# Performance work log

Measured on AMD Instinct MI355X. Metric: run time of the kernel, lower is better.

The kernel has to match this reference:

```python
import jax, jax.numpy as jnp
import numpy as np

B, N, F_IN, F_OUT, H = 4, 2048, 64, 64, 4

def setup_inputs() -> dict:
    key = jax.random.key(0)
    k1, k2, k3, k4 = jax.random.split(key, 4)
    node_features = jax.random.normal(k1, (B, N, F_IN), dtype=jnp.float32)
    adj_matrix = jax.random.randint(k2, (B, N, N), 0, 2, dtype=jnp.int32)
    # nn.Linear(in, H*out, bias=False): stored here as [in, H*out] so y = x @ W
    W = jax.random.normal(k3, (F_IN, H * F_OUT), dtype=jnp.float32) * (1.0 / np.sqrt(F_IN))
    # per-head additive-attention vector over concatenated [h_i || h_j] (width 2*F_OUT)
    attention = jax.random.normal(k4, (H, 2 * F_OUT), dtype=jnp.float32) * 0.1
    return {"node_features": node_features, "adj_matrix": adj_matrix, "W": W, "attention": attention}

def reference(node_features, adj_matrix, W, attention):
    Bv, Nv = node_features.shape[0], node_features.shape[1]
    # h: [B, H, N, F_OUT]
    h = (node_features @ W).reshape(Bv, Nv, H, F_OUT).transpose(0, 2, 1, 3)
    # Additive GAT scores: a_h . [h_i || h_j] decomposed so the [B,H,N,N,2F] concat
    # tensor is never materialized (same math as concat + einsum in the source).
    a_src, a_dst = attention[:, :F_OUT], attention[:, F_OUT:]
    s_src = jnp.einsum('bhnf,hf->bhn', h, a_src)
    s_dst = jnp.einsum('bhnf,hf->bhn', h, a_dst)
    scores = s_src[:, :, :, None] + s_dst[:, :, None, :]          # [B,H,N,N]
    scores = jnp.where(scores >= 0, scores, 0.2 * scores)          # LeakyReLU(0.2)
    mask = adj_matrix[:, None, :, :].astype(bool)                  # [B,1,N,N]
    scores = jnp.where(mask, scores, -jnp.inf)                     # masked_fill(~mask, -inf)
    attn = jax.nn.softmax(scores, axis=-1)                         # softmax over neighbors j
    # dropout is identity in eval mode (deterministic reference)
    h_prime = jnp.einsum('bhij,bhjf->bhif', attn, h)               # weighted neighbor sum
    return h_prime.transpose(0, 2, 1, 3).reshape(Bv, Nv, H * F_OUT)
```

## Files before the change

### kernel.cpp

```cpp
#include <hip/hip_runtime.h>

#define NN 2048
#define NH 4
#define COLS 256

typedef __attribute__((ext_vector_type(8))) short short8;
typedef __attribute__((ext_vector_type(4))) float f32x4;
typedef __attribute__((ext_vector_type(4))) int i32x4;
typedef __attribute__((ext_vector_type(4))) unsigned u32x4;

__device__ __forceinline__ unsigned cvtpk(float lo, float hi) {
  unsigned r;
  asm("v_cvt_pk_bf16_f32 %0, %1, %2" : "=v"(r) : "v"(lo), "v"(hi));
  return r;
}
__device__ __forceinline__ unsigned pack16(i32x4 a, i32x4 b, i32x4 c, i32x4 d) {
  unsigned m = 0;
  #pragma unroll
  for (int e = 0; e < 4; ++e) {
    m |= (a[e] != 0 ? 1u : 0u) << e;
    m |= (b[e] != 0 ? 1u : 0u) << (e + 4);
    m |= (c[e] != 0 ? 1u : 0u) << (e + 8);
    m |= (d[e] != 0 ? 1u : 0u) << (e + 12);
  }
  return m;
}

__global__ __launch_bounds__(256) void k1_prep(
    const float* __restrict__ nf, const float* __restrict__ W,
    const float* __restrict__ att, ushort* __restrict__ hB,
    float* __restrict__ s_src, float* __restrict__ s_dst)
{
  const int tid = threadIdx.x;
  const int head = tid >> 6, lane = tid & 63;
  const int bid = blockIdx.x;
  const int m0 = bid * 8;

  float w[64];
  #pragma unroll
  for (int f = 0; f < 64; ++f) w[f] = W[f * COLS + tid];

  const float LOG2E = 1.4426950408889634f;
  const float asrc = att[head * 128 + lane] * LOG2E;
  const float adst = att[head * 128 + 64 + lane] * LOG2E;

  __shared__ float xs[512];
  xs[tid]       = nf[m0 * 64 + tid];
  xs[tid + 256] = nf[m0 * 64 + 256 + tid];
  __syncthreads();

  float hv[8];
  #pragma unroll
  for (int rr = 0; rr < 8; ++rr) {
    float acc = 0.f;
    #pragma unroll
    for (int f = 0; f < 64; ++f) acc = fmaf(xs[rr * 64 + f], w[f], acc);
    hv[rr] = acc;
    float vs = acc * asrc, vd = acc * adst;
    #pragma unroll
    for (int off = 32; off > 0; off >>= 1) {
      vs += __shfl_xor(vs, off);
      vd += __shfl_xor(vd, off);
    }
    if (lane == 0) {
      const int m = m0 + rr;
      const int b = m >> 11, n = m & (NN - 1);
      s_src[(b * NH + head) * NN + n] = vs;
      s_dst[(b * NH + head) * NN + n] = vd;
    }
  }

  const int b   = m0 >> 11;
  const int n0  = m0 & (NN - 1);
  const int jc  = n0 >> 5;
  const int grp = (n0 >> 3) & 3;
  const int t   = (tid >> 4) & 3, fl = tid & 15;
  uint4 vv;
  vv.x = cvtpk(hv[0], hv[1]);
  vv.y = cvtpk(hv[2], hv[3]);
  vv.z = cvtpk(hv[4], hv[5]);
  vv.w = cvtpk(hv[6], hv[7]);
  const size_t chunk =
      (((size_t)(b * NH + head) * 64 + jc) * 4 + t) * 64 + (grp * 16 + fl);
  *(uint4*)(hB + chunk * 8) = vv;
}

__global__ __launch_bounds__(512) void k2_main(
    const int* __restrict__ adj, const ushort* __restrict__ hB,
    const float* __restrict__ s_src, const float* __restrict__ s_dst,
    float* __restrict__ out)
{
  const int tid = threadIdx.x;
  const int wv  = tid >> 6;
  const int h   = wv >> 1;
  const int js  = wv & 1;
  const int l   = tid & 63;
  const int L   = blockIdx.x;
  const int b    = (L & 7) >> 1;
  const int iblk = ((L >> 3) << 1) + (L & 1);
  const int i0   = iblk << 4;

  const int bh   = b * NH + h;
  const int r16  = l & 15;
  const int grp  = l >> 4;
  const int koff = grp << 3;

  __shared__ unsigned abits[16][65];
  __shared__ float red[NH][5][4][64];

  {
    const int srow = tid >> 5, sseg = tid & 31;
    const int* sb = adj + ((size_t)(b * NN + i0 + srow)) * NN + sseg * 64;
    unsigned m[4];
    #pragma unroll
    for (int q = 0; q < 4; ++q) {
      const i32x4 a0 = *(const i32x4*)(sb + q * 16);
      const i32x4 a1 = *(const i32x4*)(sb + q * 16 + 4);
      const i32x4 a2 = *(const i32x4*)(sb + q * 16 + 8);
      const i32x4 a3 = *(const i32x4*)(sb + q * 16 + 12);
      m[q] = pack16(a0, a1, a2, a3);
    }
    abits[srow][sseg * 2]     = m[0] | (m[1] << 16);
    abits[srow][sseg * 2 + 1] = m[2] | (m[3] << 16);
  }
  __syncthreads();

  const float ssl = s_src[bh * NN + i0 + r16];
  const float*  sdp = s_dst + bh * NN;
  const ushort* hbW = hB + (size_t)bh * 131072 + l * 8;

  const short8 ones = {(short)0x3F80, (short)0x3F80, (short)0x3F80, (short)0x3F80,
                       (short)0x3F80, (short)0x3F80, (short)0x3F80, (short)0x3F80};

  f32x4 acc[4];
  #pragma unroll
  for (int q = 0; q < 4; ++q) acc[q] = (f32x4){0.f, 0.f, 0.f, 0.f};
  f32x4 acd = (f32x4){0.f, 0.f, 0.f, 0.f};

  #pragma unroll 2
  for (int jc = js * 32; jc < js * 32 + 32; ++jc) {
    const unsigned msk = abits[r16][jc] >> koff;
    const int jb = jc * 32 + koff;
    const f32x4 sd0 = *(const f32x4*)(sdp + jb);
    const f32x4 sd1 = *(const f32x4*)(sdp + jb + 4);
    const ushort* hc = hbW + jc * 2048;
    const short8 hb0 = *(const short8*)(hc);
    const short8 hb1 = *(const short8*)(hc + 512);
    const short8 hb2 = *(const short8*)(hc + 1024);
    const short8 hb3 = *(const short8*)(hc + 1536);

    float pl[8];
    #pragma unroll
    for (int e = 0; e < 8; ++e) {
      const float sdv = (e < 4) ? sd0[e] : sd1[e - 4];
      float x = ssl + sdv;
      x = fmaxf(x, 0.2f * x);
      const float p = __builtin_amdgcn_exp2f(x);
      pl[e] = ((msk >> e) & 1u) ? p : 0.f;
    }
    u32x4 pa;
    #pragma unroll
    for (int e2 = 0; e2 < 4; ++e2) pa[e2] = cvtpk(pl[2 * e2], pl[2 * e2 + 1]);
    union { u32x4 u; short8 s; } ca; ca.u = pa;
    const short8 pal = ca.s;

    acc[0] = __builtin_amdgcn_mfma_f32_16x16x32_bf16(pal, hb0, acc[0], 0, 0, 0);
    acc[1] = __builtin_amdgcn_mfma_f32_16x16x32_bf16(pal, hb1, acc[1], 0, 0, 0);
    acc[2] = __builtin_amdgcn_mfma_f32_16x16x32_bf16(pal, hb2, acc[2], 0, 0, 0);
    acc[3] = __builtin_amdgcn_mfma_f32_16x16x32_bf16(pal, hb3, acc[3], 0, 0, 0);
    acd    = __builtin_amdgcn_mfma_f32_16x16x32_bf16(pal, ones, acd,    0, 0, 0);
  }

  if (js) {
    #pragma unroll
    for (int t = 0; t < 4; ++t)
      #pragma unroll
      for (int r = 0; r < 4; ++r) red[h][t][r][l] = acc[t][r];
    #pragma unroll
    for (int r = 0; r < 4; ++r) red[h][4][r][l] = acd[r];
  }
  __syncthreads();

  if (!js) {
    #pragma unroll
    for (int t = 0; t < 4; ++t)
      #pragma unroll
      for (int r = 0; r < 4; ++r) acc[t][r] += red[h][t][r][l];
    #pragma unroll
    for (int r = 0; r < 4; ++r) acd[r] += red[h][4][r][l];

    float rl[4];
    #pragma unroll
    for (int r = 0; r < 4; ++r) rl[r] = 1.0f / acd[r];
    #pragma unroll
    for (int t = 0; t < 4; ++t) {
      #pragma unroll
      for (int r = 0; r < 4; ++r) {
        const int i = i0 + grp * 4 + r;
        const size_t oidx = ((size_t)(b * NN + i) * COLS) + h * 64 + t * 16 + r16;
        out[oidx] = acc[t][r] * rl[r];
      }
    }
  }
}

extern "C" void kernel_launch(void* const* d_in, const int* in_sizes, int n_in,
                              void* d_out, int out_size, void* d_ws, size_t ws_size,
                              hipStream_t stream) {
  const float* nf  = (const float*)d_in[0];
  const int*   adj = (const int*)d_in[1];
  const float* W   = (const float*)d_in[2];
  const float* att = (const float*)d_in[3];

  ushort* hB    = (ushort*)d_ws;
  float*  s_src = (float*)((char*)d_ws + (size_t)16 * 64 * NN * 2);
  float*  s_dst = s_src + 16 * NN;

  hipLaunchKernelGGL(k1_prep, dim3(1024), dim3(256), 0, stream,
                     nf, W, att, hB, s_src, s_dst);
  hipLaunchKernelGGL(k2_main, dim3(512), dim3(512), 0, stream,
                     adj, hB, s_src, s_dst, (float*)d_out);
}
```

Measured before the change: 56.05 us.

## Double-buffer h tiles into LDS via async global_load_lds, drop split-j reduction

```diff
diff --git a/kernel.cpp b/kernel.cpp
--- a/kernel.cpp
+++ b/kernel.cpp
@@ -24,6 +24,11 @@
     m |= (d[e] != 0 ? 1u : 0u) << (e + 12);
   }
   return m;
+}
+__device__ __forceinline__ void gload_lds16(const void* g, void* l) {
+  __builtin_amdgcn_global_load_lds(
+      (const __attribute__((address_space(1))) void*)g,
+      (__attribute__((address_space(3))) void*)l, 16, 0, 0);
 }
 
 __global__ __launch_bounds__(256) void k1_prep(
@@ -85,19 +90,18 @@
   *(uint4*)(hB + chunk * 8) = vv;
 }
 
-__global__ __launch_bounds__(512) void k2_main(
+__global__ __launch_bounds__(256) void k2_main(
     const int* __restrict__ adj, const ushort* __restrict__ hB,
     const float* __restrict__ s_src, const float* __restrict__ s_dst,
     float* __restrict__ out)
 {
   const int tid = threadIdx.x;
-  const int wv  = tid >> 6;
-  const int h   = wv >> 1;
-  const int js  = wv & 1;
+  const int h   = tid >> 6;
   const int l   = tid & 63;
   const int L   = blockIdx.x;
-  const int b    = (L & 7) >> 1;
-  const int iblk = ((L >> 3) << 1) + (L & 1);
+  const int xcd  = L & 7, pos = L >> 3;
+  const int b    = xcd >> 1;
+  const int iblk = (xcd & 1) * 64 + pos;
   const int i0   = iblk << 4;
 
   const int bh   = b * NH + h;
@@ -105,29 +109,40 @@
   const int grp  = l >> 4;
   const int koff = grp << 3;
 
+  __shared__ ushort  hbuf[NH][2][2048];
+  __shared__ float   sdl[NH][NN];
   __shared__ unsigned abits[16][65];
-  __shared__ float red[NH][5][4][64];
 
   {
-    const int srow = tid >> 5, sseg = tid & 31;
-    const int* sb = adj + ((size_t)(b * NN + i0 + srow)) * NN + sseg * 64;
-    unsigned m[4];
-    #pragma unroll
-    for (int q = 0; q < 4; ++q) {
-      const i32x4 a0 = *(const i32x4*)(sb + q * 16);
-      const i32x4 a1 = *(const i32x4*)(sb + q * 16 + 4);
-      const i32x4 a2 = *(const i32x4*)(sb + q * 16 + 8);
-      const i32x4 a3 = *(const i32x4*)(sb + q * 16 + 12);
-      m[q] = pack16(a0, a1, a2, a3);
-    }
-    abits[srow][sseg * 2]     = m[0] | (m[1] << 16);
-    abits[srow][sseg * 2 + 1] = m[2] | (m[3] << 16);
+    const int srow = tid >> 4, sseg = tid & 15;
+    const int* sb = adj + ((size_t)(b * NN + i0 + srow)) * NN + sseg * 128;
+    #pragma unroll
+    for (int p = 0; p < 4; ++p) {
+      const i32x4 a0 = *(const i32x4*)(sb + p * 32);
+      const i32x4 a1 = *(const i32x4*)(sb + p * 32 + 4);
+      const i32x4 a2 = *(const i32x4*)(sb + p * 32 + 8);
+      const i32x4 a3 = *(const i32x4*)(sb + p * 32 + 12);
+      const i32x4 a4 = *(const i32x4*)(sb + p * 32 + 16);
+      const i32x4 a5 = *(const i32x4*)(sb + p * 32 + 20);
+      const i32x4 a6 = *(const i32x4*)(sb + p * 32 + 24);
+      const i32x4 a7 = *(const i32x4*)(sb + p * 32 + 28);
+      const unsigned lo = pack16(a0, a1, a2, a3);
+      const unsigned hi = pack16(a4, a5, a6, a7);
+      abits[srow][sseg * 4 + p] = lo | (hi << 16);
+    }
+  }
+  {
+    const int sh = tid >> 6, sc = tid & 63;
+    const float* sp = s_dst + (size_t)(b * NH + sh) * NN + sc * 32;
+    float* dp = &sdl[sh][sc * 32];
+    #pragma unroll
+    for (int k = 0; k < 8; ++k)
+      *(f32x4*)(dp + k * 4) = *(const f32x4*)(sp + k * 4);
   }
   __syncthreads();
 
   const float ssl = s_src[bh * NN + i0 + r16];
-  const float*  sdp = s_dst + bh * NN;
-  const ushort* hbW = hB + (size_t)bh * 131072 + l * 8;
+  const ushort* hbSrc = hB + (size_t)bh * 131072 + l * 8;
 
   const short8 ones = {(short)0x3F80, (short)0x3F80, (short)0x3F80, (short)0x3F80,
                        (short)0x3F80, (short)0x3F80, (short)0x3F80, (short)0x3F80};
@@ -137,17 +152,33 @@
   for (int q = 0; q < 4; ++q) acc[q] = (f32x4){0.f, 0.f, 0.f, 0.f};
   f32x4 acd = (f32x4){0.f, 0.f, 0.f, 0.f};
 
-  #pragma unroll 2
-  for (int jc = js * 32; jc < js * 32 + 32; ++jc) {
+#define STAGE(JC, BUF)                                                   \
+  {                                                                      \
+    _Pragma("unroll")                                                    \
+    for (int t = 0; t < 4; ++t)                                          \
+      gload_lds16(hbSrc + (JC) * 2048 + t * 512, &hbuf[h][(BUF)][t * 512]); \
+  }
+
+  STAGE(0, 0);
+  STAGE(1, 1);
+
+  #pragma unroll 1
+  for (int jc = 0; jc < 64; ++jc) {
+    const int buf = jc & 1;
+    asm volatile("s_waitcnt vmcnt(4)" ::: "memory");
+
+    const short8 hb0 = *(const short8*)&hbuf[h][buf][l * 8];
+    const short8 hb1 = *(const short8*)&hbuf[h][buf][512 + l * 8];
+    const short8 hb2 = *(const short8*)&hbuf[h][buf][1024 + l * 8];
+    const short8 hb3 = *(const short8*)&hbuf[h][buf][1536 + l * 8];
+    const int jb = jc * 32 + koff;
+    const f32x4 sd0 = *(const f32x4*)&sdl[h][jb];
+    const f32x4 sd1 = *(const f32x4*)&sdl[h][jb + 4];
     const unsigned msk = abits[r16][jc] >> koff;
-    const int jb = jc * 32 + koff;
-    const f32x4 sd0 = *(const f32x4*)(sdp + jb);
-    const f32x4 sd1 = *(const f32x4*)(sdp + jb + 4);
-    const ushort* hc = hbW + jc * 2048;
-    const short8 hb0 = *(const short8*)(hc);
-    const short8 hb1 = *(const short8*)(hc + 512);
-    const short8 hb2 = *(const short8*)(hc + 1024);
-    const short8 hb3 = *(const short8*)(hc + 1536);
+
+    asm volatile("s_waitcnt lgkmcnt(0)" ::: "memory");
+    __builtin_amdgcn_sched_barrier(0);
+    if (jc < 62) STAGE(jc + 2, buf);
 
     float pl[8];
     #pragma unroll
@@ -168,38 +199,20 @@
     acc[1] = __builtin_amdgcn_mfma_f32_16x16x32_bf16(pal, hb1, acc[1], 0, 0, 0);
     acc[2] = __builtin_amdgcn_mfma_f32_16x16x32_bf16(pal, hb2, acc[2], 0, 0, 0);
     acc[3] = __builtin_amdgcn_mfma_f32_16x16x32_bf16(pal, hb3, acc[3], 0, 0, 0);
-    acd    = __builtin_amdgcn_mfma_f32_16x16x32_bf16(pal, ones, acd,    0, 0, 0);
-  }
-
-  if (js) {
-    #pragma unroll
-    for (int t = 0; t < 4; ++t)
-      #pragma unroll
-      for (int r = 0; r < 4; ++r) red[h][t][r][l] = acc[t][r];
-    #pragma unroll
-    for (int r = 0; r < 4; ++r) red[h][4][r][l] = acd[r];
-  }
-  __syncthreads();
-
-  if (!js) {
-    #pragma unroll
-    for (int t = 0; t < 4; ++t)
-      #pragma unroll
-      for (int r = 0; r < 4; ++r) acc[t][r] += red[h][t][r][l];
-    #pragma unroll
-    for (int r = 0; r < 4; ++r) acd[r] += red[h][4][r][l];
-
-    float rl[4];
-    #pragma unroll
-    for (int r = 0; r < 4; ++r) rl[r] = 1.0f / acd[r];
-    #pragma unroll
-    for (int t = 0; t < 4; ++t) {
-      #pragma unroll
-      for (int r = 0; r < 4; ++r) {
-        const int i = i0 + grp * 4 + r;
-        const size_t oidx = ((size_t)(b * NN + i) * COLS) + h * 64 + t * 16 + r16;
-        out[oidx] = acc[t][r] * rl[r];
-      }
+    acd    = __builtin_amdgcn_mfma_f32_16x16x32_bf16(pal, ones,    acd,    0, 0, 0);
+  }
+#undef STAGE
+
+  float rl[4];
+  #pragma unroll
+  for (int r = 0; r < 4; ++r) rl[r] = 1.0f / acd[r];
+  #pragma unroll
+  for (int t = 0; t < 4; ++t) {
+    #pragma unroll
+    for (int r = 0; r < 4; ++r) {
+      const int i = i0 + grp * 4 + r;
+      const size_t oidx = ((size_t)(b * NN + i) * COLS) + h * 64 + t * 16 + r16;
+      out[oidx] = acc[t][r] * rl[r];
     }
   }
 }
@@ -218,6 +231,6 @@
 
   hipLaunchKernelGGL(k1_prep, dim3(1024), dim3(256), 0, stream,
                      nf, W, att, hB, s_src, s_dst);
-  hipLaunchKernelGGL(k2_main, dim3(512), dim3(512), 0, stream,
+  hipLaunchKernelGGL(k2_main, dim3(512), dim3(256), 0, stream,
                      adj, hB, s_src, s_dst, (float*)d_out);
 }
```

Result: slower. 61.31 us (+9.4%).
